# Performance work log

Hardware: AMD Instinct MI355X
Metric: run time of the kernel (lower is better)

## Reference

```python
import jax, jax.numpy as jnp
import numpy as np

B, IN_SIZE, IN_DIM = 16, 2048, 512
HEADS, OUT_SIZE = 4, 64
EPS = 0.1
MAX_ITER = 30
SIGMA = 0.1


def setup_inputs() -> dict:
    key = jax.random.key(0)
    k1, k2 = jax.random.split(key)
    x = jax.random.normal(k1, (B, IN_SIZE, IN_DIM), dtype=jnp.float32)
    stdv = 1.0 / np.sqrt(OUT_SIZE)
    weight = jax.random.uniform(k2, (HEADS, OUT_SIZE, IN_DIM), jnp.float32, -stdv, stdv)
    return {"x": x, "weight": weight}


def _position_filter(in_size, out_size, sigma):
    # 1-D gaussian position filter (image=False branch of get_position_filter)
    a = jnp.arange(0.0, in_size, dtype=jnp.float32)[:, None] / in_size
    b = jnp.arange(0.0, out_size, dtype=jnp.float32)[None, :] / out_size
    return jnp.exp(-(((a - b) / sigma) ** 2))  # (in_size, out_size)


def log_sinkhorn(K, iterations):
    """Log-domain Sinkhorn. K: (B, H, N, M) log-kernel.
    Row marginal a = 1/N (uniform, no mask). Scaling vectors are
    detached (envelope trick) before forming the transport plan,
    matching the original OTK implementation."""
    Bn, H, N, M = K.shape
    log_a = jnp.full((Bn, H, N), -jnp.log(jnp.float32(N)), dtype=K.dtype)
    u0 = jnp.zeros((Bn, H, N), K.dtype)
    v0 = jnp.zeros((Bn, H, M), K.dtype)

    def step(carry, _):
        u, v = carry
        Z = K + u[..., :, None] + v[..., None, :]
        u = log_a - jax.nn.logsumexp(Z, axis=-1)
        Z = K + u[..., :, None] + v[..., None, :]
        v = -jax.nn.logsumexp(Z, axis=-2)
        return (u, v), None

    (u, v), _ = jax.lax.scan(step, (u0, v0), None, length=iterations)
    u = jax.lax.stop_gradient(u)
    v = jax.lax.stop_gradient(v)
    return jnp.exp(K + u[..., :, None] + v[..., None, :])  # (B,H,N,M)


def reference(x, weight):
    # x: (B, N, D); weight: (H, M, D)
    pf = _position_filter(IN_SIZE, OUT_SIZE, SIGMA)  # (N, M)
    # euclidean cost via expansion (cdist)
    x2 = jnp.sum(x * x, axis=-1)                      # (B, N)
    w2 = jnp.sum(weight * weight, axis=-1)            # (H, M)
    xw = jnp.einsum('bnd,hmd->bhnm', x, weight)       # (B, H, N, M)
    C = jnp.sqrt(jnp.maximum(x2[:, None, :, None] + w2[None, :, None, :] - 2.0 * xw, 0.0))
    K = (-C / EPS) * pf[None, None]                   # position filter applied to log-kernel
    P = log_sinkhorn(K, MAX_ITER)                     # (B, H, N, M) transport plan
    # attn: (B, M, H, N) -> (B, M*H, N)
    attn = jnp.transpose(P, (0, 3, 1, 2)).reshape(B, OUT_SIZE * HEADS, IN_SIZE)
    out = jnp.matmul(attn, x)                         # (B, M*H, D)
    return out.reshape(B, OUT_SIZE, HEADS * IN_DIM)
```

## Files before the change

kernel.cpp:

```cpp
#include <hip/hip_runtime.h>
#include <hip/hip_fp16.h>


typedef _Float16 h2 __attribute__((ext_vector_type(2)));
typedef _Float16 h8 __attribute__((ext_vector_type(8)));
typedef float f4 __attribute__((ext_vector_type(4)));

#define NB 16
#define NN 2048
#define ND 512
#define NH 4
#define NM 64
#define NITER 30
#define EUSCALE 8.0f

static __device__ __forceinline__ float fdot2f(h2 a, h2 b, float c) {
#if __has_builtin(__builtin_amdgcn_fdot2)
  return __builtin_amdgcn_fdot2(a, b, c, false);
#else
  return (float)a[0] * (float)b[0] + (float)a[1] * (float)b[1] + c;
#endif
}

static __device__ __forceinline__ h2 pkrtz(float a, float b) {
  return __builtin_bit_cast(h2, __builtin_amdgcn_cvt_pkrtz(a, b));
}

static __device__ __forceinline__ h8 pack8(float4 a, float4 b) {
  h8 r;
  r[0] = (_Float16)a.x; r[1] = (_Float16)a.y; r[2] = (_Float16)a.z; r[3] = (_Float16)a.w;
  r[4] = (_Float16)b.x; r[5] = (_Float16)b.y; r[6] = (_Float16)b.z; r[7] = (_Float16)b.w;
  return r;
}

static __device__ __forceinline__ float sq4(float4 a) {
  return a.x * a.x + a.y * a.y + a.z * a.z + a.w * a.w;
}

__global__ __launch_bounds__(512) void k1_buildE(const float* __restrict__ x,
                                                 const float* __restrict__ w,
                                                 _Float16* __restrict__ E) {
  __shared__ _Float16 Ah[128][72];
  __shared__ _Float16 Bh[256][72];
  __shared__ float x2s[128][4];
  __shared__ float w2s[256][2];
  __shared__ float x2r[128];
  __shared__ float w2r[256];

  const int b = blockIdx.y;
  const int n0 = blockIdx.x * 128;
  const int tid = threadIdx.x;
  const int lane = tid & 63;
  const int wv = tid >> 6;
  const int lrow = lane & 15;
  const int kq = lane >> 4;

  f4 acc[16];
#pragma unroll
  for (int i = 0; i < 16; ++i) acc[i] = (f4){0.f, 0.f, 0.f, 0.f};

  const int ar = tid >> 2, ac = (tid & 3) * 16;
  const int br = tid >> 1, bc = (tid & 1) * 32;
  const float* xsrc = x + ((size_t)(b * NN + n0 + ar) * ND + ac);
  const float* wsrc = w + ((size_t)br * ND + bc);
  float x2p = 0.f, w2p = 0.f;

  for (int kt = 0; kt < 8; ++kt) {
    {
      const float4* s4 = (const float4*)(xsrc + kt * 64);
      float4 a0 = s4[0], a1 = s4[1], a2 = s4[2], a3 = s4[3];
      x2p += sq4(a0) + sq4(a1) + sq4(a2) + sq4(a3);
      *(h8*)&Ah[ar][ac] = pack8(a0, a1);
      *(h8*)&Ah[ar][ac + 8] = pack8(a2, a3);
    }
    {
      const float4* s4 = (const float4*)(wsrc + kt * 64);
      float4 u0 = s4[0], u1 = s4[1], u2 = s4[2], u3 = s4[3];
      float4 u4 = s4[4], u5 = s4[5], u6 = s4[6], u7 = s4[7];
      w2p += sq4(u0) + sq4(u1) + sq4(u2) + sq4(u3)
           + sq4(u4) + sq4(u5) + sq4(u6) + sq4(u7);
      *(h8*)&Bh[br][bc] = pack8(u0, u1);
      *(h8*)&Bh[br][bc + 8] = pack8(u2, u3);
      *(h8*)&Bh[br][bc + 16] = pack8(u4, u5);
      *(h8*)&Bh[br][bc + 24] = pack8(u6, u7);
    }
    __syncthreads();
#pragma unroll
    for (int s = 0; s < 2; ++s) {
      h8 af = *(const h8*)&Ah[wv * 16 + lrow][s * 32 + kq * 8];
#pragma unroll
      for (int cf = 0; cf < 16; ++cf) {
        h8 bf = *(const h8*)&Bh[cf * 16 + lrow][s * 32 + kq * 8];
        acc[cf] = __builtin_amdgcn_mfma_f32_16x16x32_f16(af, bf, acc[cf], 0, 0, 0);
      }
    }
    __syncthreads();
  }

  x2s[ar][tid & 3] = x2p;
  w2s[br][tid & 1] = w2p;
  __syncthreads();
  if (tid < 128) {
    x2r[tid] = x2s[tid][0] + x2s[tid][1] + x2s[tid][2] + x2s[tid][3];
  } else if (tid < 384) {
    const int r = tid - 128;
    w2r[r] = w2s[r][0] + w2s[r][1];
  }
  __syncthreads();

#pragma unroll
  for (int cf = 0; cf < 16; ++cf) {
    const int mg = cf * 16 + lrow;
    const int hh = mg >> 6;
    const int m = mg & 63;
    const float w2v = w2r[mg];
    const float bm = (float)m * (1.0f / 64.0f);
    _Float16* Eb = E + ((size_t)(b * NH + hh) * NN) * NM;
#pragma unroll
    for (int j = 0; j < 4; ++j) {
      const int nl = wv * 16 + kq * 4 + j;
      const int n = n0 + nl;
      const float c2 = x2r[nl] + w2v - 2.0f * acc[cf][j];
      const float Cd = sqrtf(fmaxf(c2, 0.0f));
      const float tt = (float)n * (1.0f / 2048.0f) - bm;
      const float pf = __expf(-100.0f * tt * tt);
      const float Ev = __expf(-10.0f * Cd * pf);
      Eb[(size_t)n * NM + m] = (_Float16)Ev;
    }
  }
}

__global__ __launch_bounds__(512) void k20_fused(const float* __restrict__ x,
                                                 const _Float16* __restrict__ E,
                                                 _Float16* __restrict__ xT,
                                                 _Float16* __restrict__ Pt) {
  __shared__ union {
    float tile[128][65];
    struct {
      float evf[64];
      h2 evh[32];
      unsigned int pbuf[512];
    } s2;
  } sm;
  const int bid = blockIdx.x;
  const int tid = threadIdx.x;

  if (bid >= 64) {
    auto tile = sm.tile;
    const int sub = tid >> 8;
    const int t = tid & 255;
    const int bid2 = bid - 64;
#pragma unroll
    for (int p = 0; p < 2; ++p) {
      if (p) __syncthreads();
      const int t4 = bid2 * 4 + p * 2 + sub;
      const int b = t4 >> 8;
      const int rem = t4 & 255;
      const int n0 = (rem & 31) * 64;
      const int d0 = (rem >> 5) * 64;
      const int rbase = sub << 6;
      const int nr = t >> 2;
      const int ds = (t & 3) * 16;
      const float4* src = (const float4*)(x + ((size_t)(b * NN + n0 + nr) * ND + d0 + ds));
      float4 v0 = src[0], v1 = src[1], v2 = src[2], v3 = src[3];
      float vals[16] = {v0.x, v0.y, v0.z, v0.w, v1.x, v1.y, v1.z, v1.w,
                        v2.x, v2.y, v2.z, v2.w, v3.x, v3.y, v3.z, v3.w};
#pragma unroll
      for (int j = 0; j < 16; ++j) tile[rbase + ds + j][nr] = vals[j];
      __syncthreads();
      const int dr = t >> 2;
      const int ns = (t & 3) * 16;
      h8 o0, o1;
#pragma unroll
      for (int j = 0; j < 8; ++j) o0[j] = (_Float16)tile[rbase + dr][ns + j];
#pragma unroll
      for (int j = 0; j < 8; ++j) o1[j] = (_Float16)tile[rbase + dr][ns + 8 + j];
      _Float16* dst = xT + ((size_t)(b * ND + d0 + dr) * NN + n0 + ns);
      *(h8*)dst = o0;
      *(h8*)(dst + 8) = o1;
    }
    return;
  }

  const int bh = bid;
  const int b = bh >> 2, h = bh & 3;
  const int lane = tid & 63;

  float* evf = sm.s2.evf;
  h2* evh = sm.s2.evh;
  unsigned int* pbuf = sm.s2.pbuf;

  const _Float16* Ep = E + (size_t)bh * (NN * NM);

  h2 e[4][32];
#pragma unroll
  for (int i = 0; i < 4; ++i) {
    const uint4* src = (const uint4*)(Ep + (size_t)(4 * tid + i) * NM);
#pragma unroll
    for (int q = 0; q < 8; ++q) {
      uint4 v = src[q];
      e[i][q * 4 + 0] = __builtin_bit_cast(h2, v.x);
      e[i][q * 4 + 1] = __builtin_bit_cast(h2, v.y);
      e[i][q * 4 + 2] = __builtin_bit_cast(h2, v.z);
      e[i][q * 4 + 3] = __builtin_bit_cast(h2, v.w);
    }
  }

  float eu[4] = {1.f, 1.f, 1.f, 1.f};
  if (tid < 64) evf[tid] = 1.f;
  if (tid < 32) evh[tid] = pkrtz(1.f, 1.f);
  __syncthreads();

#pragma unroll 1
  for (int it = 0; it < NITER; ++it) {
    h2 evr[32];
    {
      const uint4* ev4 = (const uint4*)evh;
#pragma unroll
      for (int q8 = 0; q8 < 8; ++q8) {
        uint4 v = ev4[q8];
        evr[q8 * 4 + 0] = __builtin_bit_cast(h2, v.x);
        evr[q8 * 4 + 1] = __builtin_bit_cast(h2, v.y);
        evr[q8 * 4 + 2] = __builtin_bit_cast(h2, v.z);
        evr[q8 * 4 + 3] = __builtin_bit_cast(h2, v.w);
      }
    }
    float sa[4] = {0.f, 0.f, 0.f, 0.f};
    float sb[4] = {0.f, 0.f, 0.f, 0.f};
#pragma unroll
    for (int q = 0; q < 16; ++q) {
#pragma unroll
      for (int i = 0; i < 4; ++i) sa[i] = fdot2f(e[i][q], evr[q], sa[i]);
    }
#pragma unroll
    for (int q = 16; q < 32; ++q) {
#pragma unroll
      for (int i = 0; i < 4; ++i) sb[i] = fdot2f(e[i][q], evr[q], sb[i]);
    }
#pragma unroll
    for (int i = 0; i < 4; ++i) {
      eu[i] = 4.8828125e-4f * __builtin_amdgcn_rcpf(eu[i] * (sa[i] + sb[i]));
    }
    h2 eup[4];
#pragma unroll
    for (int i = 0; i < 4; ++i) {
      const float es = eu[i] * EUSCALE;
      eup[i] = pkrtz(es, es);
    }
    h2 tp[32];
#pragma unroll
    for (int q = 0; q < 32; ++q) {
      tp[q] = e[0][q] * eup[0] + e[1][q] * eup[1];
      tp[q] += e[2][q] * eup[2] + e[3][q] * eup[3];
    }
#pragma unroll
    for (int k = 0; k < 5; ++k) {
      const int nn = 32 >> k;
      const bool up = (lane >> k) & 1;
#pragma unroll
      for (int p = 0; p < (nn >> 1); ++p) {
        h2 keep = up ? tp[p + (nn >> 1)] : tp[p];
        h2 send = up ? tp[p] : tp[p + (nn >> 1)];
        int rv = __shfl_xor(__builtin_bit_cast(int, send), 1 << k, 64);
        tp[p] = keep + __builtin_bit_cast(h2, rv);
      }
    }
    pbuf[tid] = __builtin_bit_cast(unsigned int, tp[0]);
    __syncthreads();
    if (tid < 32) {
      const int j = tid;
      const int rev = ((j & 1) << 4) | ((j & 2) << 2) | (j & 4) | ((j & 8) >> 2) | ((j & 16) >> 4);
      float T0 = 0.f, T1 = 0.f;
#pragma unroll
      for (int wq = 0; wq < 8; ++wq) {
        h2 a = __builtin_bit_cast(h2, pbuf[wq * 64 + rev]);
        h2 c = __builtin_bit_cast(h2, pbuf[wq * 64 + rev + 32]);
        T0 += (float)a[0] + (float)c[0];
        T1 += (float)a[1] + (float)c[1];
      }
      const float e0 = evf[2 * j], e1 = evf[2 * j + 1];
      const float n0 = EUSCALE * __builtin_amdgcn_rcpf(e0 * T0);
      const float n1 = EUSCALE * __builtin_amdgcn_rcpf(e1 * T1);
      evf[2 * j] = n0;
      evf[2 * j + 1] = n1;
      evh[j] = pkrtz(n0, n1);
    }
    __syncthreads();
  }

  _Float16* Pb = Pt + ((size_t)(b * 256 + h)) * NN;
#pragma unroll
  for (int q = 0; q < 32; ++q) {
    const float ev0 = evf[2 * q];
    const float ev1 = evf[2 * q + 1];
    float a0[4], a1[4];
#pragma unroll
    for (int i = 0; i < 4; ++i) {
      a0[i] = (float)e[i][q][0] * eu[i] * ev0;
      a1[i] = (float)e[i][q][1] * eu[i] * ev1;
    }
    uint2 st0, st1;
    st0.x = __builtin_bit_cast(unsigned int, pkrtz(a0[0], a0[1]));
    st0.y = __builtin_bit_cast(unsigned int, pkrtz(a0[2], a0[3]));
    st1.x = __builtin_bit_cast(unsigned int, pkrtz(a1[0], a1[1]));
    st1.y = __builtin_bit_cast(unsigned int, pkrtz(a1[2], a1[3]));
    *(uint2*)(Pb + (size_t)(2 * q) * 4 * NN + 4 * tid) = st0;
    *(uint2*)(Pb + (size_t)(2 * q + 1) * 4 * NN + 4 * tid) = st1;
  }
}

__global__ __launch_bounds__(256) void k3_out(const _Float16* __restrict__ Pt,
                                              const _Float16* __restrict__ xT,
                                              float* __restrict__ out) {
  __shared__ _Float16 As[64][72];
  __shared__ _Float16 Bs[64][72];
  const int b = blockIdx.z;
  const int hf = blockIdx.y;
  const int dt = blockIdx.x;
  const int tid = threadIdx.x;
  const int lane = tid & 63;
  const int wv = tid >> 6;
  const int lrow = lane & 15;
  const int kq = lane >> 4;

  f4 acc[4];
#pragma unroll
  for (int i = 0; i < 4; ++i) acc[i] = (f4){0.f, 0.f, 0.f, 0.f};

  const int ar = tid >> 2, ac = (tid & 3) * 16;
  const _Float16* asrc = Pt + ((size_t)(b * 256 + hf * 64 + ar) * NN + ac);
  const _Float16* bsrc = xT + ((size_t)(b * ND + dt * 64 + ar) * NN + ac);

  h8 a0 = *(const h8*)(asrc);
  h8 a1 = *(const h8*)(asrc + 8);
  h8 b0 = *(const h8*)(bsrc);
  h8 b1 = *(const h8*)(bsrc + 8);

  for (int kt = 0; kt < 32; ++kt) {
    *(h8*)&As[ar][ac] = a0;
    *(h8*)&As[ar][ac + 8] = a1;
    *(h8*)&Bs[ar][ac] = b0;
    *(h8*)&Bs[ar][ac + 8] = b1;
    __syncthreads();
    if (kt < 31) {
      const int k0 = (kt + 1) * 64;
      a0 = *(const h8*)(asrc + k0);
      a1 = *(const h8*)(asrc + k0 + 8);
      b0 = *(const h8*)(bsrc + k0);
      b1 = *(const h8*)(bsrc + k0 + 8);
    }
#pragma unroll
    for (int s = 0; s < 2; ++s) {
      h8 af = *(const h8*)&As[wv * 16 + lrow][s * 32 + kq * 8];
#pragma unroll
      for (int cf = 0; cf < 4; ++cf) {
        h8 bf = *(const h8*)&Bs[cf * 16 + lrow][s * 32 + kq * 8];
        acc[cf] = __builtin_amdgcn_mfma_f32_16x16x32_f16(af, bf, acc[cf], 0, 0, 0);
      }
    }
    __syncthreads();
  }
#pragma unroll
  for (int cf = 0; cf < 4; ++cf) {
    const int d = dt * 64 + cf * 16 + lrow;
#pragma unroll
    for (int j = 0; j < 4; ++j) {
      const int row = hf * 64 + wv * 16 + kq * 4 + j;
      out[(size_t)(b * 256 + row) * ND + d] = acc[cf][j];
    }
  }
}

extern "C" void kernel_launch(void* const* d_in, const int* in_sizes, int n_in,
                              void* d_out, int out_size, void* d_ws, size_t ws_size,
                              hipStream_t stream) {
  const float* x = (const float*)d_in[0];
  const float* w = (const float*)d_in[1];
  float* out = (float*)d_out;
  char* ws = (char*)d_ws;
  _Float16* xT = (_Float16*)ws;
  _Float16* E  = (_Float16*)(ws + (size_t)33554432);
  _Float16* Pt = (_Float16*)(ws + (size_t)50331648);

  k1_buildE<<<dim3(16, NB), 512, 0, stream>>>(x, w, E);
  k20_fused<<<64 + 1024, 512, 0, stream>>>(x, E, xT, Pt);
  k3_out<<<dim3(8, 4, NB), 256, 0, stream>>>(Pt, xT, out);
}
```

Baseline: 151.3 us.

## Stream E rows from global each Sinkhorn iteration instead of holding in registers

The Sinkhorn kernel stops keeping the 128 h2 registers of E per thread for the whole loop. Each iteration now reloads every row from global memory (likely L2-resident), staging it through a per-thread LDS slot so the row can be reused for the column-sum accumulation. E is reloaded once more after the loop to form the transport plan. This frees registers, but it adds 30 rounds of global and LDS traffic per block and a large dynamic shared memory allocation, which also affects the transpose blocks that share the kernel.

```diff
diff --git a/kernel.cpp b/kernel.cpp
--- a/kernel.cpp
+++ b/kernel.cpp
@@ -13,6 +13,11 @@
 #define NM 64
 #define NITER 30
 #define EUSCALE 8.0f
+
+#define ROWBUF_STRIDE 144
+#define OFF_EVF 73728
+#define OFF_EVH 73984
+#define OFF_PBUF 74048
 
 static __device__ __forceinline__ float fdot2f(h2 a, h2 b, float c) {
 #if __has_builtin(__builtin_amdgcn_fdot2)
@@ -134,19 +139,12 @@
                                                  const _Float16* __restrict__ E,
                                                  _Float16* __restrict__ xT,
                                                  _Float16* __restrict__ Pt) {
-  __shared__ union {
-    float tile[128][65];
-    struct {
-      float evf[64];
-      h2 evh[32];
-      unsigned int pbuf[512];
-    } s2;
-  } sm;
+  extern __shared__ __align__(16) char smem[];
   const int bid = blockIdx.x;
   const int tid = threadIdx.x;
 
   if (bid >= 64) {
-    auto tile = sm.tile;
+    auto tile = (float(*)[65])smem;
     const int sub = tid >> 8;
     const int t = tid & 255;
     const int bid2 = bid - 64;
@@ -186,25 +184,12 @@
   const int b = bh >> 2, h = bh & 3;
   const int lane = tid & 63;
 
-  float* evf = sm.s2.evf;
-  h2* evh = sm.s2.evh;
-  unsigned int* pbuf = sm.s2.pbuf;
+  char* slot = smem + tid * ROWBUF_STRIDE;
+  float* evf = (float*)(smem + OFF_EVF);
+  h2* evh = (h2*)(smem + OFF_EVH);
+  unsigned int* pbuf = (unsigned int*)(smem + OFF_PBUF);
 
   const _Float16* Ep = E + (size_t)bh * (NN * NM);
-
-  h2 e[4][32];
-#pragma unroll
-  for (int i = 0; i < 4; ++i) {
-    const uint4* src = (const uint4*)(Ep + (size_t)(4 * tid + i) * NM);
-#pragma unroll
-    for (int q = 0; q < 8; ++q) {
-      uint4 v = src[q];
-      e[i][q * 4 + 0] = __builtin_bit_cast(h2, v.x);
-      e[i][q * 4 + 1] = __builtin_bit_cast(h2, v.y);
-      e[i][q * 4 + 2] = __builtin_bit_cast(h2, v.z);
-      e[i][q * 4 + 3] = __builtin_bit_cast(h2, v.w);
-    }
-  }
 
   float eu[4] = {1.f, 1.f, 1.f, 1.f};
   if (tid < 64) evf[tid] = 1.f;
@@ -213,46 +198,52 @@
 
 #pragma unroll 1
   for (int it = 0; it < NITER; ++it) {
+    asm volatile("" ::: "memory");
     h2 evr[32];
     {
       const uint4* ev4 = (const uint4*)evh;
 #pragma unroll
-      for (int q8 = 0; q8 < 8; ++q8) {
-        uint4 v = ev4[q8];
-        evr[q8 * 4 + 0] = __builtin_bit_cast(h2, v.x);
-        evr[q8 * 4 + 1] = __builtin_bit_cast(h2, v.y);
-        evr[q8 * 4 + 2] = __builtin_bit_cast(h2, v.z);
-        evr[q8 * 4 + 3] = __builtin_bit_cast(h2, v.w);
-      }
-    }
-    float sa[4] = {0.f, 0.f, 0.f, 0.f};
-    float sb[4] = {0.f, 0.f, 0.f, 0.f};
-#pragma unroll
-    for (int q = 0; q < 16; ++q) {
-#pragma unroll
-      for (int i = 0; i < 4; ++i) sa[i] = fdot2f(e[i][q], evr[q], sa[i]);
-    }
-#pragma unroll
-    for (int q = 16; q < 32; ++q) {
-#pragma unroll
-      for (int i = 0; i < 4; ++i) sb[i] = fdot2f(e[i][q], evr[q], sb[i]);
-    }
-#pragma unroll
-    for (int i = 0; i < 4; ++i) {
-      eu[i] = 4.8828125e-4f * __builtin_amdgcn_rcpf(eu[i] * (sa[i] + sb[i]));
-    }
-    h2 eup[4];
-#pragma unroll
-    for (int i = 0; i < 4; ++i) {
-      const float es = eu[i] * EUSCALE;
-      eup[i] = pkrtz(es, es);
+      for (int j = 0; j < 8; ++j) {
+        uint4 v = ev4[j];
+        evr[j * 4 + 0] = __builtin_bit_cast(h2, v.x);
+        evr[j * 4 + 1] = __builtin_bit_cast(h2, v.y);
+        evr[j * 4 + 2] = __builtin_bit_cast(h2, v.z);
+        evr[j * 4 + 3] = __builtin_bit_cast(h2, v.w);
+      }
     }
     h2 tp[32];
 #pragma unroll
-    for (int q = 0; q < 32; ++q) {
-      tp[q] = e[0][q] * eup[0] + e[1][q] * eup[1];
-      tp[q] += e[2][q] * eup[2] + e[3][q] * eup[3];
-    }
+    for (int q = 0; q < 32; ++q) tp[q] = (h2){(_Float16)0.f, (_Float16)0.f};
+
+#pragma unroll
+    for (int r = 0; r < 4; ++r) {
+      const uint4* src = (const uint4*)(Ep + (size_t)(4 * tid + r) * NM);
+      float sa = 0.f, sb = 0.f, sc = 0.f, sd = 0.f;
+#pragma unroll
+      for (int j = 0; j < 8; ++j) {
+        uint4 v = src[j];
+        *(uint4*)(slot + j * 16) = v;
+        sa = fdot2f(__builtin_bit_cast(h2, v.x), evr[j * 4 + 0], sa);
+        sb = fdot2f(__builtin_bit_cast(h2, v.y), evr[j * 4 + 1], sb);
+        sc = fdot2f(__builtin_bit_cast(h2, v.z), evr[j * 4 + 2], sc);
+        sd = fdot2f(__builtin_bit_cast(h2, v.w), evr[j * 4 + 3], sd);
+      }
+      const float eun =
+          4.8828125e-4f * __builtin_amdgcn_rcpf(eu[r] * ((sa + sb) + (sc + sd)));
+      eu[r] = eun;
+      const float es = eun * EUSCALE;
+      const h2 p = pkrtz(es, es);
+      asm volatile("" ::: "memory");
+#pragma unroll
+      for (int j = 0; j < 8; ++j) {
+        uint4 v = *(const uint4*)(slot + j * 16);
+        tp[j * 4 + 0] += __builtin_bit_cast(h2, v.x) * p;
+        tp[j * 4 + 1] += __builtin_bit_cast(h2, v.y) * p;
+        tp[j * 4 + 2] += __builtin_bit_cast(h2, v.z) * p;
+        tp[j * 4 + 3] += __builtin_bit_cast(h2, v.w) * p;
+      }
+    }
+
 #pragma unroll
     for (int k = 0; k < 5; ++k) {
       const int nn = 32 >> k;
@@ -288,6 +279,20 @@
     __syncthreads();
   }
 
+  asm volatile("" ::: "memory");
+  h2 ee[4][32];
+#pragma unroll
+  for (int i = 0; i < 4; ++i) {
+    const uint4* src = (const uint4*)(Ep + (size_t)(4 * tid + i) * NM);
+#pragma unroll
+    for (int j = 0; j < 8; ++j) {
+      uint4 v = src[j];
+      ee[i][j * 4 + 0] = __builtin_bit_cast(h2, v.x);
+      ee[i][j * 4 + 1] = __builtin_bit_cast(h2, v.y);
+      ee[i][j * 4 + 2] = __builtin_bit_cast(h2, v.z);
+      ee[i][j * 4 + 3] = __builtin_bit_cast(h2, v.w);
+    }
+  }
   _Float16* Pb = Pt + ((size_t)(b * 256 + h)) * NN;
 #pragma unroll
   for (int q = 0; q < 32; ++q) {
@@ -296,8 +301,8 @@
     float a0[4], a1[4];
 #pragma unroll
     for (int i = 0; i < 4; ++i) {
-      a0[i] = (float)e[i][q][0] * eu[i] * ev0;
-      a1[i] = (float)e[i][q][1] * eu[i] * ev1;
+      a0[i] = (float)ee[i][q][0] * eu[i] * ev0;
+      a1[i] = (float)ee[i][q][1] * eu[i] * ev1;
     }
     uint2 st0, st1;
     st0.x = __builtin_bit_cast(unsigned int, pkrtz(a0[0], a0[1]));
@@ -382,7 +387,10 @@
   _Float16* E  = (_Float16*)(ws + (size_t)33554432);
   _Float16* Pt = (_Float16*)(ws + (size_t)50331648);
 
+  (void)hipFuncSetAttribute((const void*)k20_fused,
+                            hipFuncAttributeMaxDynamicSharedMemorySize, 76800);
+
   k1_buildE<<<dim3(16, NB), 512, 0, stream>>>(x, w, E);
-  k20_fused<<<64 + 1024, 512, 0, stream>>>(x, E, xT, Pt);
+  k20_fused<<<64 + 1024, 512, 76096, stream>>>(x, E, xT, Pt);
   k3_out<<<dim3(8, 4, NB), 256, 0, stream>>>(Pt, xT, out);
 }
```

After: 362.1 us. 2.39x slower.
